# Optimization experiments

Measured on AMD Instinct MI355X. Metric: run time of the kernel, lower is better.

The kernel has to match this reference:

```python
import jax, jax.numpy as jnp
import numpy as np

N_VIS, N_ASSOC, N_MOTOR, IN_DIM, T = 8192, 4096, 1024, 4096, 16
TAU_MEM, V_TH, TAU_ELIG = 20.0, 1.0, 500.0


def setup_inputs() -> dict:
    key = jax.random.key(0)
    ks = jax.random.split(key, 8)
    visual_input = jax.random.uniform(ks[0], (T, IN_DIM), dtype=jnp.float32)
    noise = jax.random.uniform(ks[1], (T, N_VIS), dtype=jnp.float32)  # replaces torch.rand_like
    dopamine = jax.random.normal(ks[2], (T,), dtype=jnp.float32)
    # visual_encoder: nn.Linear(4096, n_visual) default init (kaiming-uniform-ish); use small uniform
    lim = 1.0 / np.sqrt(IN_DIM)
    W_enc = jax.random.uniform(ks[3], (N_VIS, IN_DIM), minval=-lim, maxval=lim, dtype=jnp.float32)
    b_enc = jax.random.uniform(ks[4], (N_VIS,), minval=-lim, maxval=lim, dtype=jnp.float32)
    # v_to_a / a_to_m: uniform_(0.01, 0.05), no bias
    W_va = jax.random.uniform(ks[5], (N_ASSOC, N_VIS), minval=0.01, maxval=0.05, dtype=jnp.float32)
    W_am = jax.random.uniform(ks[6], (N_MOTOR, N_ASSOC), minval=0.01, maxval=0.05, dtype=jnp.float32)
    return {"visual_input": visual_input, "noise": noise, "dopamine": dopamine,
            "W_enc": W_enc, "b_enc": b_enc, "W_va": W_va, "W_am": W_am}


def reference(visual_input, noise, dopamine, W_enc, b_enc, W_va, W_am):
    decay_m = 1.0 - 1.0 / TAU_MEM
    decay_e = 1.0 - 1.0 / TAU_ELIG
    f32 = jnp.float32

    def step(carry, xs):
        vV, vA, vM, eVA, eAM, Wva, Wam = carry
        x, u, d = xs
        # visual encoding + Bernoulli spikes
        rates = jax.nn.sigmoid(x @ W_enc.T + b_enc)             # [n_visual]
        in_spk = (u < rates * 0.3).astype(f32)
        # LIF: visual layer
        vV = vV * decay_m + in_spk
        v_spk = (vV > V_TH).astype(f32)
        vV = vV * (1.0 - v_spk)
        # LIF: assoc layer
        vA = vA * decay_m + (v_spk @ Wva.T) * 0.1
        a_spk = (vA > V_TH).astype(f32)
        vA = vA * (1.0 - a_spk)
        # LIF: motor layer
        vM = vM * decay_m + (a_spk @ Wam.T) * 0.1
        m_spk = (vM > V_TH).astype(f32)
        vM = vM * (1.0 - m_spk)
        # DA-STDP eligibility traces (rank-1 updates)
        eVA = eVA * decay_e + jnp.outer(v_spk, a_spk) * 0.01    # [n_visual, n_assoc]
        eAM = eAM * decay_e + jnp.outer(a_spk, m_spk) * 0.01    # [n_assoc, n_motor]
        # conditional dopamine-gated weight update
        gate = jnp.abs(d) > 0.1
        Wva_new = jnp.clip(Wva + jnp.clip(d * eVA.T * 0.1, -0.01, 0.01), 0.0, 1.0)
        Wam_new = jnp.clip(Wam + jnp.clip(d * eAM.T * 0.1, -0.01, 0.01), 0.0, 1.0)
        Wva = jnp.where(gate, Wva_new, Wva)
        Wam = jnp.where(gate, Wam_new, Wam)
        eVA = jnp.where(gate, eVA * 0.5, eVA)
        eAM = jnp.where(gate, eAM * 0.5, eAM)
        return (vV, vA, vM, eVA, eAM, Wva, Wam), m_spk

    init = (jnp.zeros(N_VIS, f32), jnp.zeros(N_ASSOC, f32), jnp.zeros(N_MOTOR, f32),
            jnp.zeros((N_VIS, N_ASSOC), f32), jnp.zeros((N_ASSOC, N_MOTOR), f32),
            W_va, W_am)
    _, motor_spikes = jax.lax.scan(step, init, (visual_input, noise, dopamine))
    return motor_spikes  # [T, n_motor]
```

## Files before the change

kernel.cpp:

```cpp
#include <hip/hip_runtime.h>
#include <cstdint>

#define N_VIS   8192
#define N_ASSOC 4096
#define N_MOTOR 1024
#define IN_DIM  4096
#define T_STEPS 16

template<int COLS, int CS>
__global__ __launch_bounds__(512, 4) void mv_rowwave_kernel(
        const float* __restrict__ Wg, const float* __restrict__ Vg,
        float* __restrict__ Sp, int nrows) {
    constexpr int F4PR = COLS / 4;
    constexpr int SEG4 = F4PR / CS;
    constexpr int NIT  = SEG4 / 64;
    __shared__ float4 vs[2][16 * 64];
    const int tid  = threadIdx.x;
    const int lane = tid & 63, wv = tid >> 6;
    const int rb   = blockIdx.x / CS;
    const int sp   = blockIdx.x % CS;
    const int j0   = rb * 16 + wv * 2;
    const float4* W4a = (const float4*)Wg + (size_t)j0 * F4PR + (size_t)sp * SEG4;
    const float4* W4b = W4a + F4PR;
    const float4* V4  = (const float4*)Vg + (size_t)sp * SEG4;

    float acc[2][T_STEPS];
#pragma unroll
    for (int t = 0; t < T_STEPS; ++t) { acc[0][t] = 0.f; acc[1][t] = 0.f; }

    {
        int f = tid;
#pragma unroll
        for (int p = 0; p < 2; ++p, f += 512) {
            int t = f >> 6, c = f & 63;
            vs[0][f] = V4[(size_t)t * F4PR + c];
        }
    }
    float4 wa = W4a[lane], wb = W4b[lane];
    __syncthreads();

    int buf = 0;
#pragma unroll 1
    for (int it = 0; it < NIT; ++it) {
        float4 wan = wa, wbn = wb;
        if (it + 1 < NIT) {
            wan = W4a[(it + 1) * 64 + lane];
            wbn = W4b[(it + 1) * 64 + lane];
            int f = tid;
#pragma unroll
            for (int p = 0; p < 2; ++p, f += 512) {
                int t = f >> 6, c = f & 63;
                vs[buf ^ 1][f] = V4[(size_t)t * F4PR + (it + 1) * 64 + c];
            }
        }
#pragma unroll
        for (int t = 0; t < T_STEPS; ++t) {
            float4 v = vs[buf][t * 64 + lane];
            acc[0][t] = fmaf(wa.x, v.x, acc[0][t]);
            acc[0][t] = fmaf(wa.y, v.y, acc[0][t]);
            acc[0][t] = fmaf(wa.z, v.z, acc[0][t]);
            acc[0][t] = fmaf(wa.w, v.w, acc[0][t]);
            acc[1][t] = fmaf(wb.x, v.x, acc[1][t]);
            acc[1][t] = fmaf(wb.y, v.y, acc[1][t]);
            acc[1][t] = fmaf(wb.z, v.z, acc[1][t]);
            acc[1][t] = fmaf(wb.w, v.w, acc[1][t]);
        }
        __syncthreads();
        wa = wan; wb = wbn; buf ^= 1;
    }

#pragma unroll
    for (int t = 0; t < T_STEPS; ++t) {
        float a0 = acc[0][t], a1 = acc[1][t];
        for (int o = 32; o; o >>= 1) {
            a0 += __shfl_down(a0, o, 64);
            a1 += __shfl_down(a1, o, 64);
        }
        acc[0][t] = a0; acc[1][t] = a1;
    }
    if (lane == 0) {
#pragma unroll
        for (int r = 0; r < 2; ++r) {
            float4* So = (float4*)(Sp + ((size_t)sp * nrows + j0 + r) * 16);
#pragma unroll
            for (int q = 0; q < 4; ++q)
                So[q] = make_float4(acc[r][q*4], acc[r][q*4+1], acc[r][q*4+2], acc[r][q*4+3]);
        }
    }
}

__global__ __launch_bounds__(256) void vlif_kernel(
        const float* __restrict__ S1, const float* __restrict__ noise,
        const float* __restrict__ b, unsigned* __restrict__ vmask,
        float* __restrict__ V) {
    const int i = blockIdx.x * 256 + threadIdx.x;
    float a[T_STEPS];
#pragma unroll
    for (int t = 0; t < T_STEPS; ++t) a[t] = S1[(size_t)i * 16 + t];
    const float bb = b[i];
    float v = 0.f;
    unsigned msk = 0;
#pragma unroll
    for (int t = 0; t < T_STEPS; ++t) {
        float logit = a[t] + bb;
        float rate = 1.0f / (1.0f + expf(-logit));
        float u = noise[t * N_VIS + i];
        float ins = (u < rate * 0.3f) ? 1.0f : 0.0f;
        v = v * 0.95f + ins;
        if (v > 1.0f) { msk |= (1u << t); v = 0.f; }
    }
    vmask[i] = msk;
#pragma unroll
    for (int t = 0; t < T_STEPS; ++t)
        V[t * N_VIS + i] = (float)((msk >> t) & 1u);
}

__global__ void ktab_kernel(const float* __restrict__ dop, float* __restrict__ K,
                            int* __restrict__ ovl_z) {
    __shared__ float C[256];
    __shared__ float sd[16];
    __shared__ unsigned sg[16];
    const int p = threadIdx.x;
    ovl_z[p] = 0; ovl_z[p + 256] = 0;
    if (p < 16) {
        float d = dop[p];
        sd[p] = d;
        sg[p] = (fabsf(d) > 0.1f) ? 1u : 0u;
    }
    __syncthreads();
    {
        const int s = p >> 4, r = p & 15;
        float c = 0.f;
        if (s >= r) {
            c = 1.f;
            for (int u = r; u < s; ++u) {
                if (sg[u]) c *= 0.5f;
                c *= 0.998f;
            }
        }
        C[p] = c;
    }
    __syncthreads();
    {
        const int t = p >> 4, r = p & 15;
        float kk = 0.f;
        for (int s = r; s < t; ++s)
            if (sg[s]) kk += ((sd[s] * 0.1f) * 0.01f) * C[s * 16 + r];
        K[p] = kk;
    }
}

__global__ void ovl_kernel(const unsigned* __restrict__ mask, int words_per_block,
                           int* __restrict__ ovl) {
    const int p = threadIdx.x;
    const int r = p >> 4, t = p & 15;
    const unsigned* w = mask + blockIdx.x * words_per_block;
    int c = 0;
    for (int i = 0; i < words_per_block; ++i)
        c += (int)((w[i] >> r) & (w[i] >> t) & 1u);
    atomicAdd(&ovl[p], c);
}

__global__ __launch_bounds__(64) void rec_kernel(
        const float* __restrict__ base, const int* __restrict__ ovl,
        const float* __restrict__ K, unsigned* __restrict__ mask_out,
        float* __restrict__ outp, int out_stride,
        float* __restrict__ outV, int n_rows, int cs) {
    __shared__ float KO[256];
    const int tid = threadIdx.x;
    for (int p = tid; p < 256; p += 64) {
        const int t = p >> 4, r = p & 15;
        KO[p] = K[p] * (float)ovl[r * 16 + t];
    }
    __syncthreads();

    const int j = blockIdx.x * 64 + tid;
    float br[T_STEPS];
#pragma unroll
    for (int t = 0; t < T_STEPS; ++t) br[t] = base[(size_t)j * 16 + t];
#pragma unroll 1
    for (int s = 1; s < cs; ++s)
#pragma unroll
        for (int t = 0; t < T_STEPS; ++t)
            br[t] += base[((size_t)s * n_rows + j) * 16 + t];

    float vmem = 0.f;
    unsigned am = 0;
#pragma unroll
    for (int t = 0; t < T_STEPS; ++t) {
        float I = br[t];
        for (int r = 0; r < t; ++r)
            if ((am >> r) & 1u) I += KO[t * 16 + r];
        vmem = vmem * 0.95f + I * 0.1f;
        const bool s = vmem > 1.0f;
        if (s) { vmem = 0.f; am |= (1u << t); }
        if (outp) outp[t * out_stride + j] = s ? 1.0f : 0.0f;
    }
    mask_out[j] = am;
    if (outV) {
#pragma unroll
        for (int t = 0; t < T_STEPS; ++t)
            outV[t * n_rows + j] = (float)((am >> t) & 1u);
    }
}

extern "C" void kernel_launch(void* const* d_in, const int* in_sizes, int n_in,
                              void* d_out, int out_size, void* d_ws, size_t ws_size,
                              hipStream_t stream) {
    const float* x     = (const float*)d_in[0];
    const float* noise = (const float*)d_in[1];
    const float* dop   = (const float*)d_in[2];
    const float* W_enc = (const float*)d_in[3];
    const float* b_enc = (const float*)d_in[4];
    const float* W_va  = (const float*)d_in[5];
    const float* W_am  = (const float*)d_in[6];
    float* out = (float*)d_out;
    (void)in_sizes; (void)n_in; (void)out_size; (void)ws_size;

    char* ws = (char*)d_ws;
    size_t off = 0;
    unsigned* vmask = (unsigned*)(ws + off); off += N_VIS * 4;
    unsigned* amask = (unsigned*)(ws + off); off += N_ASSOC * 4;
    unsigned* mmask = (unsigned*)(ws + off); off += N_MOTOR * 4;
    float*    K     = (float*)(ws + off);    off += 256 * 4;
    int*      ovl_v = (int*)(ws + off);      off += 256 * 4;
    int*      ovl_a = (int*)(ws + off);      off += 256 * 4;
    float*    S1    = (float*)(ws + off);    off += (size_t)N_VIS * 16 * 4;
    float*    S2    = (float*)(ws + off);    off += (size_t)2 * N_ASSOC * 16 * 4;
    float*    S3    = (float*)(ws + off);    off += (size_t)4 * N_MOTOR * 16 * 4;
    float*    Vv    = (float*)(ws + off);    off += (size_t)T_STEPS * N_VIS * 4;
    float*    Va    = (float*)(ws + off);    off += (size_t)T_STEPS * N_ASSOC * 4;

    ktab_kernel<<<1, 256, 0, stream>>>(dop, K, ovl_v);
    mv_rowwave_kernel<IN_DIM, 1><<<N_VIS / 16, 512, 0, stream>>>(W_enc, x, S1, N_VIS);
    vlif_kernel<<<N_VIS / 256, 256, 0, stream>>>(S1, noise, b_enc, vmask, Vv);
    ovl_kernel<<<32, 256, 0, stream>>>(vmask, N_VIS / 32, ovl_v);
    mv_rowwave_kernel<N_VIS, 2><<<(N_ASSOC / 16) * 2, 512, 0, stream>>>(W_va, Vv, S2, N_ASSOC);
    rec_kernel<<<N_ASSOC / 64, 64, 0, stream>>>(S2, ovl_v, K, amask, nullptr, 0, Va, N_ASSOC, 2);
    ovl_kernel<<<16, 256, 0, stream>>>(amask, N_ASSOC / 16, ovl_a);
    mv_rowwave_kernel<N_ASSOC, 4><<<(N_MOTOR / 16) * 4, 512, 0, stream>>>(W_am, Va, S3, N_MOTOR);
    rec_kernel<<<N_MOTOR / 64, 64, 0, stream>>>(S3, ovl_a, K, mmask, out, N_MOTOR, nullptr, 0, 4);
}
```

Measured before the change: 145.3 us.

## Feed spike bitmasks directly into matvecs and raise split-K for encoder

Adds a matvec kernel that reads the per-neuron 16-bit spike masks and expands them to 0/1 floats in registers, instead of reading dense float spike matrices staged through shared memory. This removes the writes of the dense Vv/Va spike arrays, their re-reads, and the shared-memory double buffering. The encoder and W_va matvecs also get more column splits, so more blocks run and vlif/rec sum the extra partials. The cost is extra ALU work for bit extraction, plus more partial-sum traffic.

```diff
diff --git a/kernel.cpp b/kernel.cpp
--- a/kernel.cpp
+++ b/kernel.cpp
@@ -89,14 +89,76 @@
     }
 }
 
+template<int COLS, int CS>
+__global__ __launch_bounds__(512, 4) void mv_bits_kernel(
+        const float* __restrict__ Wg, const unsigned* __restrict__ mask,
+        float* __restrict__ Sp, int nrows) {
+    constexpr int F4PR = COLS / 4;
+    constexpr int SEG4 = F4PR / CS;
+    constexpr int NIT  = SEG4 / 64;
+    const int lane = threadIdx.x & 63, wv = threadIdx.x >> 6;
+    const int rb   = blockIdx.x / CS;
+    const int sp   = blockIdx.x % CS;
+    const int j0   = rb * 16 + wv * 2;
+    const float4* W4a = (const float4*)Wg + (size_t)j0 * F4PR + (size_t)sp * SEG4;
+    const float4* W4b = W4a + F4PR;
+    const uint4*  M4  = (const uint4*)mask + (size_t)sp * SEG4;
+
+    float acc0[T_STEPS], acc1[T_STEPS];
+#pragma unroll
+    for (int t = 0; t < T_STEPS; ++t) { acc0[t] = 0.f; acc1[t] = 0.f; }
+
+#pragma unroll 2
+    for (int it = 0; it < NIT; ++it) {
+        const int idx = it * 64 + lane;
+        float4 wa = W4a[idx];
+        float4 wb = W4b[idx];
+        uint4  m  = M4[idx];
+#pragma unroll
+        for (int t = 0; t < T_STEPS; ++t) {
+            float bx = (float)((m.x >> t) & 1u);
+            float by = (float)((m.y >> t) & 1u);
+            float bz = (float)((m.z >> t) & 1u);
+            float bw = (float)((m.w >> t) & 1u);
+            acc0[t] = fmaf(wa.x, bx, acc0[t]);
+            acc0[t] = fmaf(wa.y, by, acc0[t]);
+            acc0[t] = fmaf(wa.z, bz, acc0[t]);
+            acc0[t] = fmaf(wa.w, bw, acc0[t]);
+            acc1[t] = fmaf(wb.x, bx, acc1[t]);
+            acc1[t] = fmaf(wb.y, by, acc1[t]);
+            acc1[t] = fmaf(wb.z, bz, acc1[t]);
+            acc1[t] = fmaf(wb.w, bw, acc1[t]);
+        }
+    }
+
+#pragma unroll
+    for (int t = 0; t < T_STEPS; ++t) {
+        float a0 = acc0[t], a1 = acc1[t];
+        for (int o = 32; o; o >>= 1) {
+            a0 += __shfl_down(a0, o, 64);
+            a1 += __shfl_down(a1, o, 64);
+        }
+        acc0[t] = a0; acc1[t] = a1;
+    }
+    if (lane == 0) {
+        float4* So0 = (float4*)(Sp + ((size_t)sp * nrows + j0) * 16);
+        float4* So1 = (float4*)(Sp + ((size_t)sp * nrows + j0 + 1) * 16);
+#pragma unroll
+        for (int q = 0; q < 4; ++q) {
+            So0[q] = make_float4(acc0[q*4], acc0[q*4+1], acc0[q*4+2], acc0[q*4+3]);
+            So1[q] = make_float4(acc1[q*4], acc1[q*4+1], acc1[q*4+2], acc1[q*4+3]);
+        }
+    }
+}
+
 __global__ __launch_bounds__(256) void vlif_kernel(
-        const float* __restrict__ S1, const float* __restrict__ noise,
-        const float* __restrict__ b, unsigned* __restrict__ vmask,
-        float* __restrict__ V) {
+        const float* __restrict__ S1p, const float* __restrict__ noise,
+        const float* __restrict__ b, unsigned* __restrict__ vmask) {
     const int i = blockIdx.x * 256 + threadIdx.x;
     float a[T_STEPS];
 #pragma unroll
-    for (int t = 0; t < T_STEPS; ++t) a[t] = S1[(size_t)i * 16 + t];
+    for (int t = 0; t < T_STEPS; ++t)
+        a[t] = S1p[(size_t)i * 16 + t] + S1p[((size_t)N_VIS + i) * 16 + t];
     const float bb = b[i];
     float v = 0.f;
     unsigned msk = 0;
@@ -110,9 +172,6 @@
         if (v > 1.0f) { msk |= (1u << t); v = 0.f; }
     }
     vmask[i] = msk;
-#pragma unroll
-    for (int t = 0; t < T_STEPS; ++t)
-        V[t * N_VIS + i] = (float)((msk >> t) & 1u);
 }
 
 __global__ void ktab_kernel(const float* __restrict__ dop, float* __restrict__ K,
@@ -164,8 +223,7 @@
 __global__ __launch_bounds__(64) void rec_kernel(
         const float* __restrict__ base, const int* __restrict__ ovl,
         const float* __restrict__ K, unsigned* __restrict__ mask_out,
-        float* __restrict__ outp, int out_stride,
-        float* __restrict__ outV, int n_rows, int cs) {
+        float* __restrict__ outp, int out_stride, int n_rows, int cs) {
     __shared__ float KO[256];
     const int tid = threadIdx.x;
     for (int p = tid; p < 256; p += 64) {
@@ -197,11 +255,6 @@
         if (outp) outp[t * out_stride + j] = s ? 1.0f : 0.0f;
     }
     mask_out[j] = am;
-    if (outV) {
-#pragma unroll
-        for (int t = 0; t < T_STEPS; ++t)
-            outV[t * n_rows + j] = (float)((am >> t) & 1u);
-    }
 }
 
 extern "C" void kernel_launch(void* const* d_in, const int* in_sizes, int n_in,
@@ -225,19 +278,17 @@
     float*    K     = (float*)(ws + off);    off += 256 * 4;
     int*      ovl_v = (int*)(ws + off);      off += 256 * 4;
     int*      ovl_a = (int*)(ws + off);      off += 256 * 4;
-    float*    S1    = (float*)(ws + off);    off += (size_t)N_VIS * 16 * 4;
-    float*    S2    = (float*)(ws + off);    off += (size_t)2 * N_ASSOC * 16 * 4;
+    float*    S1    = (float*)(ws + off);    off += (size_t)2 * N_VIS   * 16 * 4;
+    float*    S2    = (float*)(ws + off);    off += (size_t)4 * N_ASSOC * 16 * 4;
     float*    S3    = (float*)(ws + off);    off += (size_t)4 * N_MOTOR * 16 * 4;
-    float*    Vv    = (float*)(ws + off);    off += (size_t)T_STEPS * N_VIS * 4;
-    float*    Va    = (float*)(ws + off);    off += (size_t)T_STEPS * N_ASSOC * 4;
 
     ktab_kernel<<<1, 256, 0, stream>>>(dop, K, ovl_v);
-    mv_rowwave_kernel<IN_DIM, 1><<<N_VIS / 16, 512, 0, stream>>>(W_enc, x, S1, N_VIS);
-    vlif_kernel<<<N_VIS / 256, 256, 0, stream>>>(S1, noise, b_enc, vmask, Vv);
+    mv_rowwave_kernel<IN_DIM, 2><<<(N_VIS / 16) * 2, 512, 0, stream>>>(W_enc, x, S1, N_VIS);
+    vlif_kernel<<<N_VIS / 256, 256, 0, stream>>>(S1, noise, b_enc, vmask);
     ovl_kernel<<<32, 256, 0, stream>>>(vmask, N_VIS / 32, ovl_v);
-    mv_rowwave_kernel<N_VIS, 2><<<(N_ASSOC / 16) * 2, 512, 0, stream>>>(W_va, Vv, S2, N_ASSOC);
-    rec_kernel<<<N_ASSOC / 64, 64, 0, stream>>>(S2, ovl_v, K, amask, nullptr, 0, Va, N_ASSOC, 2);
+    mv_bits_kernel<N_VIS, 4><<<(N_ASSOC / 16) * 4, 512, 0, stream>>>(W_va, vmask, S2, N_ASSOC);
+    rec_kernel<<<N_ASSOC / 64, 64, 0, stream>>>(S2, ovl_v, K, amask, nullptr, 0, N_ASSOC, 4);
     ovl_kernel<<<16, 256, 0, stream>>>(amask, N_ASSOC / 16, ovl_a);
-    mv_rowwave_kernel<N_ASSOC, 4><<<(N_MOTOR / 16) * 4, 512, 0, stream>>>(W_am, Va, S3, N_MOTOR);
-    rec_kernel<<<N_MOTOR / 64, 64, 0, stream>>>(S3, ovl_a, K, mmask, out, N_MOTOR, nullptr, 0, 4);
-}
+    mv_bits_kernel<N_ASSOC, 4><<<(N_MOTOR / 16) * 4, 512, 0, stream>>>(W_am, amask, S3, N_MOTOR);
+    rec_kernel<<<N_MOTOR / 64, 64, 0, stream>>>(S3, ovl_a, K, mmask, out, N_MOTOR, N_MOTOR, 4);
+}
```

Result: slower. 151.6 us (+4.4%).
